# Kernel tuning notes

Hardware: AMD Instinct MI355X
Metric: run time of the kernel (lower is better)

The kernel has to match this reference:

```python
import jax, jax.numpy as jnp
import numpy as np

# Fixed canonical tree batching: complete binary tree, depth D, 2^D - 1 internal nodes.
O, P_, D = 64, 64, 6          # num_obs, num_particles, tree depth
H, OBS, SD, AD = 100, 100, 8, 10  # hidden, obs_emb, sample_emb, address_emb dims
IN = OBS + SD + AD            # GRUCell input dim = 118
N = 2 ** D - 1                # internal nodes per tree


def setup_inputs() -> dict:
    key = jax.random.key(0)
    ks = jax.random.split(key, 13)
    f = lambda k, s: jax.random.normal(k, s, dtype=jnp.float32)
    return {
        "obs_embeddings": f(ks[0], (O, OBS)),
        "sample_emb": f(ks[1], (O, P_, N, SD)),
        "addr_emb": f(ks[2], (O, P_, N, AD)),
        "W_ih": f(ks[3], (3 * H, IN)) * 0.1,
        "W_hh": f(ks[4], (3 * H, H)) * 0.1,
        "b_ih": f(ks[5], (3 * H,)) * 0.1,
        "b_hh": f(ks[6], (3 * H,)) * 0.1,
        "W1": f(ks[7], (50, H)) * 0.1,
        "b1": f(ks[8], (50,)) * 0.1,
        "W2": f(ks[9], (25, 50)) * 0.1,
        "b2": f(ks[10], (25,)) * 0.1,
        "W3": f(ks[11], (1, 25)) * 0.1,
        "b3": f(ks[12], (1,)) * 0.1,
    }


def reference(obs_embeddings, sample_emb, addr_emb, W_ih, W_hh, b_ih, b_hh,
              W1, b1, W2, b2, W3, b3):
    def gru_cell(x, h):
        # torch.nn.GRUCell math
        gi = x @ W_ih.T + b_ih
        gh = h @ W_hh.T + b_hh
        i_r, i_z, i_n = jnp.split(gi, 3, axis=-1)
        h_r, h_z, h_n = jnp.split(gh, 3, axis=-1)
        r = jax.nn.sigmoid(i_r + h_r)
        z = jax.nn.sigmoid(i_z + h_z)
        n = jnp.tanh(i_n + r * h_n)
        return (1.0 - z) * n + z * h

    # Leaves (terminals) contribute zero hidden state, per the torch code.
    h_child = jnp.zeros((O, P_, 2 ** (D - 1), H), dtype=sample_emb.dtype)
    h = h_child
    # Bottom-up over levels (root = level 0). Level l has 2^l nodes,
    # occupying flat indices [2^l - 1, 2^(l+1) - 2].
    for l in range(D - 1, -1, -1):
        w = 2 ** l
        s = w - 1
        obs_b = jnp.broadcast_to(obs_embeddings[:, None, None, :], (O, P_, w, OBS))
        x = jnp.concatenate(
            [obs_b, sample_emb[:, :, s:s + w], addr_emb[:, :, s:s + w]], axis=-1)
        h = gru_cell(x, h_child)  # [O, P_, w, H]
        if l > 0:
            # Parent hidden input = sum of its two children's embeddings.
            h_child = h.reshape(O, P_, w // 2, 2, H).sum(axis=3)
    root = h[:, :, 0, :]  # [O, P_, H]
    y = jax.nn.relu(root @ W1.T + b1)
    y = jax.nn.relu(y @ W2.T + b2)
    c = (y @ W3.T + b3)[..., 0]  # [O, P_]
    return jax.nn.logsumexp(c, axis=1) - jnp.log(jnp.float32(P_))
```

## Files before the change

### kernel.cpp

```cpp
#include <hip/hip_runtime.h>
#include <hip/hip_bf16.h>

typedef __attribute__((ext_vector_type(8))) short bf16x8;
typedef __attribute__((ext_vector_type(4))) float f32x4;

__device__ __forceinline__ float sigmoidf_(float x){ return 1.0f/(1.0f+__expf(-x)); }
__device__ __forceinline__ float tanhf_(float x){ return 1.0f - 2.0f/(1.0f+__expf(2.0f*x)); }
__device__ __forceinline__ unsigned short f2bf(float f){
    __hip_bfloat16 b = __float2bfloat16(f);
    return *reinterpret_cast<unsigned short*>(&b);
}
__device__ __forceinline__ float bf2f(unsigned short u){
    __hip_bfloat16 b = *reinterpret_cast<__hip_bfloat16*>(&u);
    return __bfloat162float(b);
}
__device__ __forceinline__ void gload_lds16(const void* gsrc, void* ldst){
    __builtin_amdgcn_global_load_lds(
        (const __attribute__((address_space(1))) unsigned int*)gsrc,
        (__attribute__((address_space(3))) unsigned int*)ldst,
        16, 0, 0);
}

__global__ __launch_bounds__(64) void precompute_kernel(
    const float* __restrict__ obs, const float* __restrict__ W_ih,
    const float* __restrict__ W_hh, const float* __restrict__ b_ih,
    const float* __restrict__ b_hh, const float* __restrict__ W1,
    const float* __restrict__ W2,
    unsigned short* __restrict__ Bg,
    float* __restrict__ W1T, float* __restrict__ W2T)
{
    int t = blockIdx.x * 64 + threadIdx.x;
    if (t < 688128) {
        int o = t / 10752, r = t % 10752;
        int s = r / 512, r2 = r % 512;
        int j = r2 / 32, kk = r2 % 32;
        int region = s / 7;
        int u = (s % 7) * 16 + j;
        float wv = 0.f;
        if (u < 100) {
            int gate = region * 100 + u;
            if (kk < 18) {
                wv = W_ih[(size_t)gate * 118 + 100 + kk];
            } else if (kk == 18) {
                wv = b_ih[gate] + (region < 2 ? b_hh[gate] : 0.f);
                const float* orow = obs + o * 100;
                const float* wrow = W_ih + (size_t)gate * 118;
                for (int k = 0; k < 100; ++k) wv = fmaf(orow[k], wrow[k], wv);
            }
        }
        unsigned short h = f2bf(wv);
        unsigned short l = f2bf(wv - bf2f(h));
        int qr = kk >> 3, e = kk & 7;
        size_t base = (size_t)o * 21504 + (size_t)((s * 4 + qr) * 16 + j) * 8 + e;
        Bg[base] = h;
        Bg[base + 10752] = l;
        return;
    }
    t -= 688128;
    if (t < 43008) {
        int ks = 1 + t / 10752, r = t % 10752;
        int s = r / 512, r2 = r % 512;
        int j = r2 / 32, kk = r2 % 32;
        int tt = (s < 14) ? s : s + 7;
        int region = tt / 7;
        int u = (tt % 7) * 16 + j;
        float wv = 0.f;
        if (u < 100) {
            int gate = (region == 3 ? 2 : region) * 100 + u;
            int kh = (ks - 1) * 32 + kk;
            if (kh < 100) wv = W_hh[(size_t)gate * 100 + kh];
        }
        int qr = kk >> 3, e = kk & 7;
        size_t base = (size_t)1376256 + (size_t)(ks - 1) * 10752
                    + (size_t)((s * 4 + qr) * 16 + j) * 8 + e;
        Bg[base] = f2bf(wv);
        return;
    }
    t -= 43008;
    if (t < 5000) { int g = t / 50, j = t % 50; W1T[t] = W1[j * 100 + g]; return; }
    t -= 5000;
    if (t < 1250) { int j = t / 25, i = t % 25; W2T[t] = W2[i * 50 + j]; }
}

template<int LW1, bool LEAF1, bool LAST>
__global__ __launch_bounds__(512) void fused_pair(
    const unsigned short* __restrict__ Bg,
    const float* __restrict__ bhh,
    const float* __restrict__ samp,
    const float* __restrict__ addr,
    const unsigned short* __restrict__ hin,
    unsigned short* __restrict__ hout)
{
    extern __shared__ unsigned short smem[];
    unsigned short* B0   = smem;
    unsigned short* BH   = smem + 21504;
    unsigned short* hmid = smem + 64512;

    const int tid = threadIdx.x;
    const int lane = tid & 63;
    const int wid = tid >> 6;
    const int j15 = lane & 15;
    const int qr = lane >> 4;
    const int wk = (blockIdx.x & 7) * (gridDim.x >> 3) + (blockIdx.x >> 3);
    const int c0 = wk * 128;
    const int c0w = c0 + wid * 16;
    const int o = c0 >> (LW1 + 6);

    {
        const char* g0 = (const char*)(Bg + (size_t)o * 21504);
        const char* gH = (const char*)(Bg + 1376256);
        char* l0 = (char*)B0;
        char* lH = (char*)BH;
        #pragma unroll
        for (int it = 0; it < 16; ++it) {
            const int base = it * 512 + wid * 64;
            if (it == 15 && wid >= 6) break;
            if (base < 2688) {
                gload_lds16(g0 + (size_t)(base + lane) * 16, l0 + (size_t)base * 16);
            } else {
                const int hb = base - 2688;
                gload_lds16(gH + (size_t)(hb + lane) * 16, lH + (size_t)hb * 16);
            }
        }
    }

    f32x4 acc[28];
    #pragma unroll
    for (int t = 0; t < 28; ++t) acc[t] = (f32x4){0.f, 0.f, 0.f, 0.f};

    bf16x8 axhi, axlo;
    {
        const int w = 1 << LW1;
        const int cm = c0w + j15;
        const int opm = cm >> LW1;
        const int nodem = w - 1 + (cm & (w - 1));
        const size_t nb = (size_t)opm * 63 + nodem;
        float xv0=0.f,xv1=0.f,xv2=0.f,xv3=0.f,xv4=0.f,xv5=0.f,xv6=0.f,xv7=0.f;
        if (qr == 0) {
            const float4* s4 = (const float4*)(samp + nb * 8);
            float4 a = s4[0], b = s4[1];
            xv0=a.x; xv1=a.y; xv2=a.z; xv3=a.w; xv4=b.x; xv5=b.y; xv6=b.z; xv7=b.w;
        } else if (qr == 1) {
            const float2* a2 = (const float2*)(addr + nb * 10);
            float2 e0=a2[0], e1=a2[1], e2=a2[2], e3=a2[3];
            xv0=e0.x; xv1=e0.y; xv2=e1.x; xv3=e1.y; xv4=e2.x; xv5=e2.y; xv6=e3.x; xv7=e3.y;
        } else if (qr == 2) {
            xv0 = addr[nb * 10 + 8]; xv1 = addr[nb * 10 + 9];
            xv2 = 1.0f;
        }
        #define CVT(e, val) { unsigned short hh = f2bf(val); \
            axhi[e] = (short)hh; axlo[e] = (short)f2bf((val) - bf2f(hh)); }
        CVT(0, xv0) CVT(1, xv1) CVT(2, xv2) CVT(3, xv3)
        CVT(4, xv4) CVT(5, xv5) CVT(6, xv6) CVT(7, xv7)
        #undef CVT
    }
    bf16x8 ah1[4];
    if constexpr (!LEAF1) {
        const size_t arow = (size_t)(c0w + j15) * 128 + qr * 8;
        #pragma unroll
        for (int m = 0; m < 4; ++m)
            ah1[m] = *(const bf16x8*)(hin + arow + m * 32);
    }
    __syncthreads();

    #pragma unroll
    for (int s = 0; s < 21; ++s) {
        const unsigned short* bb = B0 + ((s * 4 + qr) * 16 + j15) * 8;
        bf16x8 bhi = *(const bf16x8*)bb;
        bf16x8 blo = *(const bf16x8*)(bb + 10752);
        acc[s] = __builtin_amdgcn_mfma_f32_16x16x32_bf16(axhi, bhi, acc[s], 0, 0, 0);
        acc[s] = __builtin_amdgcn_mfma_f32_16x16x32_bf16(axlo, bhi, acc[s], 0, 0, 0);
        acc[s] = __builtin_amdgcn_mfma_f32_16x16x32_bf16(axhi, blo, acc[s], 0, 0, 0);
    }
    if constexpr (!LEAF1) {
        #pragma unroll
        for (int ks = 1; ks <= 4; ++ks) {
            const unsigned short* hp = BH + (ks - 1) * 10752;
            #pragma unroll
            for (int s = 0; s < 21; ++s) {
                const int d = (s < 14) ? s : s + 7;
                bf16x8 bhi = *(const bf16x8*)(hp + ((s * 4 + qr) * 16 + j15) * 8);
                acc[d] = __builtin_amdgcn_mfma_f32_16x16x32_bf16(ah1[ks - 1], bhi, acc[d], 0, 0, 0);
            }
        }
    }

    #pragma unroll
    for (int t = 0; t < 7; ++t) {
        const int u = t * 16 + j15;
        const float bh = (u < 100) ? bhh[200 + u] : 0.f;
        float hv0, hv1, hv2, hv3;
        #define GATE(reg, hvout) { \
            float rr = sigmoidf_(acc[t][reg]); \
            float zz = sigmoidf_(acc[t + 7][reg]); \
            float nn = tanhf_(acc[t + 14][reg] + rr * (acc[t + 21][reg] + bh)); \
            float hcv = 0.f; \
            if constexpr (!LEAF1) \
                hcv = bf2f(hin[(size_t)(c0w + qr * 4 + reg) * 128 + u]); \
            hvout = nn + zz * (hcv - nn); }
        GATE(0, hv0) GATE(1, hv1) GATE(2, hv2) GATE(3, hv3)
        #undef GATE
        const int r0 = wid * 8 + qr * 2;
        hmid[(r0)     * 136 + u] = f2bf(hv0 + hv1);
        hmid[(r0 + 1) * 136 + u] = f2bf(hv2 + hv3);
    }
    for (int f = tid; f < 1024; f += 512)
        hmid[(f >> 4) * 136 + 112 + (f & 15)] = 0;
    __syncthreads();

    {
        constexpr int LW2 = LW1 - 1;
        const int c20 = c0 >> 1;
        const int c2w = c20 + wid * 16;
        if (wid >= 4) return;

        #pragma unroll
        for (int t = 0; t < 28; ++t) acc[t] = (f32x4){0.f, 0.f, 0.f, 0.f};

        bf16x8 axhi2, axlo2;
        {
            const int w = 1 << LW2;
            const int cm = c2w + j15;
            const int opm = cm >> LW2;
            const int nodem = w - 1 + (cm & (w - 1));
            const size_t nb = (size_t)opm * 63 + nodem;
            float xv0=0.f,xv1=0.f,xv2=0.f,xv3=0.f,xv4=0.f,xv5=0.f,xv6=0.f,xv7=0.f;
            if (qr == 0) {
                const float4* s4 = (const float4*)(samp + nb * 8);
                float4 a = s4[0], b = s4[1];
                xv0=a.x; xv1=a.y; xv2=a.z; xv3=a.w; xv4=b.x; xv5=b.y; xv6=b.z; xv7=b.w;
            } else if (qr == 1) {
                const float2* a2 = (const float2*)(addr + nb * 10);
                float2 e0=a2[0], e1=a2[1], e2=a2[2], e3=a2[3];
                xv0=e0.x; xv1=e0.y; xv2=e1.x; xv3=e1.y; xv4=e2.x; xv5=e2.y; xv6=e3.x; xv7=e3.y;
            } else if (qr == 2) {
                xv0 = addr[nb * 10 + 8]; xv1 = addr[nb * 10 + 9];
                xv2 = 1.0f;
            }
            #define CVT(e, val) { unsigned short hh = f2bf(val); \
                axhi2[e] = (short)hh; axlo2[e] = (short)f2bf((val) - bf2f(hh)); }
            CVT(0, xv0) CVT(1, xv1) CVT(2, xv2) CVT(3, xv3)
            CVT(4, xv4) CVT(5, xv5) CVT(6, xv6) CVT(7, xv7)
            #undef CVT
        }

        #pragma unroll
        for (int s = 0; s < 21; ++s) {
            const unsigned short* bb = B0 + ((s * 4 + qr) * 16 + j15) * 8;
            bf16x8 bhi = *(const bf16x8*)bb;
            bf16x8 blo = *(const bf16x8*)(bb + 10752);
            acc[s] = __builtin_amdgcn_mfma_f32_16x16x32_bf16(axhi2, bhi, acc[s], 0, 0, 0);
            acc[s] = __builtin_amdgcn_mfma_f32_16x16x32_bf16(axlo2, bhi, acc[s], 0, 0, 0);
            acc[s] = __builtin_amdgcn_mfma_f32_16x16x32_bf16(axhi2, blo, acc[s], 0, 0, 0);
        }
        #pragma unroll
        for (int ks = 1; ks <= 4; ++ks) {
            bf16x8 ahi = *(const bf16x8*)(hmid + (wid * 16 + j15) * 136
                                               + (ks - 1) * 32 + qr * 8);
            const unsigned short* hp = BH + (ks - 1) * 10752;
            #pragma unroll
            for (int s = 0; s < 21; ++s) {
                const int d = (s < 14) ? s : s + 7;
                bf16x8 bhi = *(const bf16x8*)(hp + ((s * 4 + qr) * 16 + j15) * 8);
                acc[d] = __builtin_amdgcn_mfma_f32_16x16x32_bf16(ahi, bhi, acc[d], 0, 0, 0);
            }
        }

        #pragma unroll
        for (int t = 0; t < 7; ++t) {
            const int u = t * 16 + j15;
            const float bh = (u < 100) ? bhh[200 + u] : 0.f;
            float hv0, hv1, hv2, hv3;
            #define GATE(reg, hvout) { \
                float rr = sigmoidf_(acc[t][reg]); \
                float zz = sigmoidf_(acc[t + 7][reg]); \
                float nn = tanhf_(acc[t + 14][reg] + rr * (acc[t + 21][reg] + bh)); \
                float hcv = bf2f(hmid[(wid * 16 + qr * 4 + reg) * 136 + u]); \
                hvout = nn + zz * (hcv - nn); }
            GATE(0, hv0) GATE(1, hv1) GATE(2, hv2) GATE(3, hv3)
            #undef GATE
            if (LAST) {
                unsigned short* r0 = hout + (size_t)(c2w + qr * 4) * 128 + u;
                r0[0]   = f2bf(hv0);
                r0[128] = f2bf(hv1);
                r0[256] = f2bf(hv2);
                r0[384] = f2bf(hv3);
            } else {
                unsigned short* r0 = hout + (size_t)((c2w >> 1) + qr * 2) * 128 + u;
                r0[0]   = f2bf(hv0 + hv1);
                r0[128] = f2bf(hv2 + hv3);
            }
        }
        const int u2 = 112 + j15;
        if (LAST) {
            #pragma unroll
            for (int reg = 0; reg < 4; ++reg)
                hout[(size_t)(c2w + qr * 4 + reg) * 128 + u2] = 0;
        } else {
            #pragma unroll
            for (int p = 0; p < 2; ++p)
                hout[(size_t)((c2w >> 1) + qr * 2 + p) * 128 + u2] = 0;
        }
    }
}

__global__ __launch_bounds__(256) void mlp_lse(
    const unsigned short* __restrict__ h0,
    const float* __restrict__ W1T,
    const float* __restrict__ b1,
    const float* __restrict__ W2T,
    const float* __restrict__ b2,
    const float* __restrict__ W3,
    const float* __restrict__ b3,
    float* __restrict__ out)
{
    __shared__ float hs[64 * 101];
    __shared__ float w1s[5008];
    __shared__ float w2s[1250];
    __shared__ float y1s[64 * 50];

    const int o = blockIdx.x;
    const int tid = threadIdx.x;
    const int lane = tid & 63;
    const int wid = tid >> 6;

    for (int f = tid; f < 6400; f += 256) {
        int cl = f / 100, g = f - cl * 100;
        hs[cl * 101 + g] = bf2f(h0[(size_t)(o * 64 + cl) * 128 + g]);
    }
    for (int f = tid; f < 5000; f += 256) w1s[f] = W1T[f];
    for (int f = tid; f < 1250; f += 256) w2s[f] = W2T[f];
    __syncthreads();

    const int jbase = wid * 13;
    const int jn = (wid < 3) ? 13 : 11;
    float y1[13];
    #pragma unroll
    for (int jj = 0; jj < 13; ++jj) y1[jj] = b1[jbase + jj < 50 ? jbase + jj : 49];
    #pragma unroll 2
    for (int g = 0; g < 100; ++g) {
        float rg = hs[lane * 101 + g];
        const float* wr = w1s + g * 50 + jbase;
        #pragma unroll
        for (int jj = 0; jj < 13; ++jj) y1[jj] = fmaf(rg, wr[jj], y1[jj]);
    }
    #pragma unroll
    for (int jj = 0; jj < 13; ++jj)
        if (jj < jn) y1s[lane * 50 + jbase + jj] = y1[jj];
    __syncthreads();
    if (wid != 0) return;

    const int p = lane;
    float y2[25];
    #pragma unroll
    for (int i = 0; i < 25; ++i) y2[i] = b2[i];
    #pragma unroll 2
    for (int j = 0; j < 50; ++j) {
        float v = fmaxf(y1s[p * 50 + j], 0.0f);
        const float* wr = w2s + j * 25;
        #pragma unroll
        for (int i = 0; i < 25; ++i) y2[i] = fmaf(v, wr[i], y2[i]);
    }

    float cv = b3[0];
    #pragma unroll
    for (int i = 0; i < 25; ++i) cv = fmaf(fmaxf(y2[i], 0.0f), W3[i], cv);

    float m = cv;
    #pragma unroll
    for (int s = 1; s < 64; s <<= 1) m = fmaxf(m, __shfl_xor(m, s));
    float e = __expf(cv - m);
    #pragma unroll
    for (int s = 1; s < 64; s <<= 1) e += __shfl_xor(e, s);
    if (p == 0) out[o] = m + __logf(e) - 4.1588830833596715f;
}

extern "C" void kernel_launch(void* const* d_in, const int* in_sizes, int n_in,
                              void* d_out, int out_size, void* d_ws, size_t ws_size,
                              hipStream_t stream)
{
    const float* obs  = (const float*)d_in[0];
    const float* samp = (const float*)d_in[1];
    const float* addr = (const float*)d_in[2];
    const float* W_ih = (const float*)d_in[3];
    const float* W_hh = (const float*)d_in[4];
    const float* b_ih = (const float*)d_in[5];
    const float* b_hh = (const float*)d_in[6];
    const float* W1   = (const float*)d_in[7];
    const float* b1   = (const float*)d_in[8];
    const float* W2   = (const float*)d_in[9];
    const float* b2   = (const float*)d_in[10];
    const float* W3   = (const float*)d_in[11];
    const float* b3   = (const float*)d_in[12];
    float* out = (float*)d_out;

    float* ws = (float*)d_ws;
    unsigned short* Bg = (unsigned short*)ws;
    float* W1T = ws + 709632;
    float* W2T = ws + 714632;
    unsigned short* hU1 = (unsigned short*)(ws + 715888);
    unsigned short* hU2 = (unsigned short*)(ws + 2813040);
    unsigned short* hU3 = (unsigned short*)(ws + 3337328);

    const int DYN_LDS = 146432;
    (void)hipFuncSetAttribute((const void*)fused_pair<5, true, false>,
        hipFuncAttributeMaxDynamicSharedMemorySize, DYN_LDS);
    (void)hipFuncSetAttribute((const void*)fused_pair<3, false, false>,
        hipFuncAttributeMaxDynamicSharedMemorySize, DYN_LDS);
    (void)hipFuncSetAttribute((const void*)fused_pair<1, false, true>,
        hipFuncAttributeMaxDynamicSharedMemorySize, DYN_LDS);

    precompute_kernel<<<(737386 + 63) / 64, 64, 0, stream>>>(
        obs, W_ih, W_hh, b_ih, b_hh, W1, W2, Bg, W1T, W2T);

    fused_pair<5, true, false><<<1024, 512, DYN_LDS, stream>>>(
        Bg, b_hh, samp, addr, nullptr, hU1);
    fused_pair<3, false, false><<<256, 512, DYN_LDS, stream>>>(
        Bg, b_hh, samp, addr, hU1, hU2);
    fused_pair<1, false, true><<<64, 512, DYN_LDS, stream>>>(
        Bg, b_hh, samp, addr, hU2, hU3);

    mlp_lse<<<64, 256, 0, stream>>>(hU3, W1T, b1, W2T, b2, W3, b3, out);
}
```

Measured before the change: 140.1 us.

## Drop bf16 low-part weight split for input projection, keep split bias

The input-side weights (sample/address embeddings) are now stored only as a single bf16 value, with the fused bias/obs term split into hi and lo halves across two input lanes paired with a constant 1.0 input. This removes one of three MFMAs per input tile, halves the per-observation weight buffer, and shrinks the LDS footprint and global-to-LDS copy. In exchange, the input weights lose their low-order correction, which reduces accuracy of the input projection.

Measured after the change: 132.7 us. -5.3%, faster.

```diff
diff --git a/kernel.cpp b/kernel.cpp
--- a/kernel.cpp
+++ b/kernel.cpp
@@ -36,24 +36,22 @@
         int j = r2 / 32, kk = r2 % 32;
         int region = s / 7;
         int u = (s % 7) * 16 + j;
-        float wv = 0.f;
+        unsigned short outv = 0;
         if (u < 100) {
             int gate = region * 100 + u;
             if (kk < 18) {
-                wv = W_ih[(size_t)gate * 118 + 100 + kk];
-            } else if (kk == 18) {
-                wv = b_ih[gate] + (region < 2 ? b_hh[gate] : 0.f);
+                outv = f2bf(W_ih[(size_t)gate * 118 + 100 + kk]);
+            } else if (kk == 18 || kk == 19) {
+                float bias = b_ih[gate] + (region < 2 ? b_hh[gate] : 0.f);
                 const float* orow = obs + o * 100;
                 const float* wrow = W_ih + (size_t)gate * 118;
-                for (int k = 0; k < 100; ++k) wv = fmaf(orow[k], wrow[k], wv);
+                for (int k = 0; k < 100; ++k) bias = fmaf(orow[k], wrow[k], bias);
+                if (kk == 18) outv = f2bf(bias);
+                else          outv = f2bf(bias - bf2f(f2bf(bias)));
             }
         }
-        unsigned short h = f2bf(wv);
-        unsigned short l = f2bf(wv - bf2f(h));
         int qr = kk >> 3, e = kk & 7;
-        size_t base = (size_t)o * 21504 + (size_t)((s * 4 + qr) * 16 + j) * 8 + e;
-        Bg[base] = h;
-        Bg[base + 10752] = l;
+        Bg[(size_t)o * 10752 + (size_t)((s * 4 + qr) * 16 + j) * 8 + e] = outv;
         return;
     }
     t -= 688128;
@@ -71,12 +69,16 @@
             if (kh < 100) wv = W_hh[(size_t)gate * 100 + kh];
         }
         int qr = kk >> 3, e = kk & 7;
-        size_t base = (size_t)1376256 + (size_t)(ks - 1) * 10752
-                    + (size_t)((s * 4 + qr) * 16 + j) * 8 + e;
-        Bg[base] = f2bf(wv);
+        Bg[(size_t)688128 + (size_t)(ks - 1) * 10752
+           + (size_t)((s * 4 + qr) * 16 + j) * 8 + e] = f2bf(wv);
         return;
     }
     t -= 43008;
+    if (t < 512) {
+        Bg[731136 + t] = 0;
+        return;
+    }
+    t -= 512;
     if (t < 5000) { int g = t / 50, j = t % 50; W1T[t] = W1[j * 100 + g]; return; }
     t -= 5000;
     if (t < 1250) { int j = t / 25, i = t % 25; W2T[t] = W2[i * 50 + j]; }
@@ -93,8 +95,8 @@
 {
     extern __shared__ unsigned short smem[];
     unsigned short* B0   = smem;
-    unsigned short* BH   = smem + 21504;
-    unsigned short* hmid = smem + 64512;
+    unsigned short* BH   = smem + 10752;
+    unsigned short* hmid = smem + 54272;
 
     const int tid = threadIdx.x;
     const int lane = tid & 63;
@@ -107,20 +109,21 @@
     const int o = c0 >> (LW1 + 6);
 
     {
-        const char* g0 = (const char*)(Bg + (size_t)o * 21504);
-        const char* gH = (const char*)(Bg + 1376256);
-        char* l0 = (char*)B0;
-        char* lH = (char*)BH;
-        #pragma unroll
-        for (int it = 0; it < 16; ++it) {
+        const char* g0 = (const char*)(Bg + (size_t)o * 10752);
+        const char* gH = (const char*)(Bg + 688128);
+        char* l0 = (char*)smem;
+        #pragma unroll
+        for (int it = 0; it < 13; ++it) {
             const int base = it * 512 + wid * 64;
-            if (it == 15 && wid >= 6) break;
-            if (base < 2688) {
-                gload_lds16(g0 + (size_t)(base + lane) * 16, l0 + (size_t)base * 16);
-            } else {
-                const int hb = base - 2688;
-                gload_lds16(gH + (size_t)(hb + lane) * 16, lH + (size_t)hb * 16);
-            }
+            const int fi = base + lane;
+            const char* src = (fi < 1344) ? g0 + (size_t)fi * 16
+                                          : gH + (size_t)(fi - 1344) * 16;
+            gload_lds16(src, l0 + (size_t)base * 16);
+        }
+        if (wid < 2) {
+            const int base = 6656 + wid * 64;
+            const int fi = base + lane;
+            gload_lds16(gH + (size_t)(fi - 1344) * 16, l0 + (size_t)base * 16);
         }
     }
 
@@ -147,6 +150,7 @@
         } else if (qr == 2) {
             xv0 = addr[nb * 10 + 8]; xv1 = addr[nb * 10 + 9];
             xv2 = 1.0f;
+            xv3 = 1.0f;
         }
         #define CVT(e, val) { unsigned short hh = f2bf(val); \
             axhi[e] = (short)hh; axlo[e] = (short)f2bf((val) - bf2f(hh)); }
@@ -165,12 +169,9 @@
 
     #pragma unroll
     for (int s = 0; s < 21; ++s) {
-        const unsigned short* bb = B0 + ((s * 4 + qr) * 16 + j15) * 8;
-        bf16x8 bhi = *(const bf16x8*)bb;
-        bf16x8 blo = *(const bf16x8*)(bb + 10752);
+        bf16x8 bhi = *(const bf16x8*)(B0 + ((s * 4 + qr) * 16 + j15) * 8);
         acc[s] = __builtin_amdgcn_mfma_f32_16x16x32_bf16(axhi, bhi, acc[s], 0, 0, 0);
         acc[s] = __builtin_amdgcn_mfma_f32_16x16x32_bf16(axlo, bhi, acc[s], 0, 0, 0);
-        acc[s] = __builtin_amdgcn_mfma_f32_16x16x32_bf16(axhi, blo, acc[s], 0, 0, 0);
     }
     if constexpr (!LEAF1) {
         #pragma unroll
@@ -236,6 +237,7 @@
             } else if (qr == 2) {
                 xv0 = addr[nb * 10 + 8]; xv1 = addr[nb * 10 + 9];
                 xv2 = 1.0f;
+                xv3 = 1.0f;
             }
             #define CVT(e, val) { unsigned short hh = f2bf(val); \
                 axhi2[e] = (short)hh; axlo2[e] = (short)f2bf((val) - bf2f(hh)); }
@@ -246,12 +248,9 @@
 
         #pragma unroll
         for (int s = 0; s < 21; ++s) {
-            const unsigned short* bb = B0 + ((s * 4 + qr) * 16 + j15) * 8;
-            bf16x8 bhi = *(const bf16x8*)bb;
-            bf16x8 blo = *(const bf16x8*)(bb + 10752);
+            bf16x8 bhi = *(const bf16x8*)(B0 + ((s * 4 + qr) * 16 + j15) * 8);
             acc[s] = __builtin_amdgcn_mfma_f32_16x16x32_bf16(axhi2, bhi, acc[s], 0, 0, 0);
             acc[s] = __builtin_amdgcn_mfma_f32_16x16x32_bf16(axlo2, bhi, acc[s], 0, 0, 0);
-            acc[s] = __builtin_amdgcn_mfma_f32_16x16x32_bf16(axhi2, blo, acc[s], 0, 0, 0);
         }
         #pragma unroll
         for (int ks = 1; ks <= 4; ++ks) {
@@ -396,13 +395,13 @@
 
     float* ws = (float*)d_ws;
     unsigned short* Bg = (unsigned short*)ws;
-    float* W1T = ws + 709632;
-    float* W2T = ws + 714632;
-    unsigned short* hU1 = (unsigned short*)(ws + 715888);
-    unsigned short* hU2 = (unsigned short*)(ws + 2813040);
-    unsigned short* hU3 = (unsigned short*)(ws + 3337328);
-
-    const int DYN_LDS = 146432;
+    float* W1T = ws + 365824;
+    float* W2T = ws + 370824;
+    unsigned short* hU1 = (unsigned short*)(ws + 372080);
+    unsigned short* hU2 = (unsigned short*)(ws + 2469232);
+    unsigned short* hU3 = (unsigned short*)(ws + 2993520);
+
+    const int DYN_LDS = 125952;
     (void)hipFuncSetAttribute((const void*)fused_pair<5, true, false>,
         hipFuncAttributeMaxDynamicSharedMemorySize, DYN_LDS);
     (void)hipFuncSetAttribute((const void*)fused_pair<3, false, false>,
@@ -410,7 +409,7 @@
     (void)hipFuncSetAttribute((const void*)fused_pair<1, false, true>,
         hipFuncAttributeMaxDynamicSharedMemorySize, DYN_LDS);
 
-    precompute_kernel<<<(737386 + 63) / 64, 64, 0, stream>>>(
+    precompute_kernel<<<(737898 + 63) / 64, 64, 0, stream>>>(
         obs, W_ih, W_hh, b_ih, b_hh, W1, W2, Bg, W1T, W2T);
 
     fused_pair<5, true, false><<<1024, 512, DYN_LDS, stream>>>(
```
